# Kernel optimization log

Hardware: AMD Instinct MI355X
Metric: run time of the kernel (lower is better)

Reference implementation:

```python
import jax, jax.numpy as jnp
import numpy as np
from jax import lax

C_DIM = 64
N_HEADS = 8
PATCH = 3
PAD = (PATCH - 1) // 2
EPS = 1e-6


def _unfold(x, p, pad):
    # x: [B,C,H,W] -> [B, C*p*p, H*W], torch.F.unfold ordering (C slowest, then ph, pw)
    B, C, H, W = x.shape
    xp = jnp.pad(x, ((0, 0), (0, 0), (pad, pad), (pad, pad)))
    cols = jnp.stack([xp[:, :, i:i + H, j:j + W] for i in range(p) for j in range(p)], axis=2)
    return cols.reshape(B, C * p * p, H * W)


def _fold(cols, p, pad, H, W):
    # cols: [B, C*p*p, H*W] -> [B,C,H,W] via col2im scatter-add (torch.F.fold)
    B = cols.shape[0]
    C = cols.shape[1] // (p * p)
    cols = cols.reshape(B, C, p * p, H, W)
    out = jnp.zeros((B, C, H + 2 * pad, W + 2 * pad), cols.dtype)
    for i in range(p):
        for j in range(p):
            out = out.at[:, :, i:i + H, j:j + W].add(cols[:, :, i * p + j])
    return out[:, :, pad:pad + H, pad:pad + W]


def _linear_attn(q, k, v):
    # q,k,v: [B, h, N, d]; non-softmax linear attention with ReLU features
    kv = jnp.einsum('bhnd,bhne->bhde', k, v)          # [B,h,d,d]
    ksum = k.sum(axis=2)                              # [B,h,d]
    denom = jnp.einsum('bhnd,bhd->bhn', q, ksum) + EPS
    out = jnp.einsum('bhnd,bhde->bhne', q, kv) / denom[..., None]
    return out


def setup_inputs() -> dict:
    key = jax.random.key(0)
    ks = jax.random.split(key, 5)
    B, C, H, W = 4, C_DIM, 128, 128
    x = jax.random.normal(ks[0], (B, C, H, W), jnp.float32)
    w_qkv = jax.random.normal(ks[1], (3 * C, C), jnp.float32) * 0.05
    b_qkv = jax.random.normal(ks[2], (3 * C,), jnp.float32) * 0.01
    w_proj = jax.random.normal(ks[3], (C, C, 3, 3), jnp.float32) * 0.05
    b_proj = jax.random.normal(ks[4], (C,), jnp.float32) * 0.01
    return {"x": x, "w_qkv": w_qkv, "b_qkv": b_qkv, "w_proj": w_proj, "b_proj": b_proj}


def reference(x, w_qkv, b_qkv, w_proj, b_proj):
    B, C, H, W = x.shape
    p, pad, h = PATCH, PAD, N_HEADS
    N = H * W
    # 1x1 conv qkv
    qkv = jnp.einsum('bchw,oc->bohw', x, w_qkv) + b_qkv[None, :, None, None]
    q, k, v = qkv[:, :C], qkv[:, C:2 * C], qkv[:, 2 * C:]
    q = jax.nn.relu(q)
    k = jax.nn.relu(k)
    # im2col: [B, C*p*p, N]
    qc = _unfold(q, p, pad)
    kc = _unfold(k, p, pad)
    vc = _unfold(v, p, pad)
    d = (C * p * p) // h
    qh = qc.reshape(B, h, d, N).transpose(0, 1, 3, 2)  # [B,h,N,d]
    kh = kc.reshape(B, h, d, N).transpose(0, 1, 3, 2)
    vh = vc.reshape(B, h, d, N).transpose(0, 1, 3, 2)
    o = _linear_attn(qh, kh, vh)                       # [B,h,N,d]
    oc = o.transpose(0, 1, 3, 2).reshape(B, C * p * p, N)
    folded = _fold(oc, p, pad, H, W)
    ones_cols = _unfold(jnp.ones((B, C, H, W), x.dtype), p, pad)
    counts = _fold(ones_cols, p, pad, H, W)
    y = folded / counts
    # 3x3 proj conv
    y = lax.conv_general_dilated(y, w_proj, (1, 1), [(1, 1), (1, 1)],
                                 dimension_numbers=('NCHW', 'OIHW', 'NCHW'))
    y = y + b_proj[None, :, None, None]
    return y
```

## Files before the change

kernel.cpp:

```cpp
#include <hip/hip_runtime.h>

#define BB 4
#define CC 64
#define HH 128
#define WW 128
#define NN (HH*WW)
#define HP 130
#define NPP (HP*HP)
#define HPS 136
#define VROWS 132
#define NPPS (VROWS*HPS)
#define HP2 132
#define NPP2 (HP2*HP2)
#define NH 8
#define DD 72

__global__ __launch_bounds__(256) void k0_wt(const float* __restrict__ wproj, float* __restrict__ wt){
    int idx = blockIdx.x*256 + threadIdx.x;
    if (idx >= 64*9*64) return;
    int oc = idx & 63;
    int w  = (idx >> 6) % 9;
    int ci = idx / 576;
    wt[idx] = wproj[(oc*64 + ci)*9 + w];
}

__global__ __launch_bounds__(256) void k1_qkv(const float* __restrict__ x,
        const float* __restrict__ wqkv, const float* __restrict__ bqkv,
        float* __restrict__ Qp, float* __restrict__ Kp, float* __restrict__ Vp){
    __shared__ float wl[64*68];
    __shared__ float bl[64];
    const int t = threadIdx.x;
    const int gy = blockIdx.y;
    const int b  = blockIdx.z;
    for (int k = 0; k < 16; ++k){
        int idx = t + k*256;
        int orel = idx >> 6, c = idx & 63;
        wl[c*68 + orel] = wqkv[(gy*64 + orel)*64 + c];
    }
    if (t < 64) bl[t] = bqkv[gy*64 + t];
    __syncthreads();
    const int pix = blockIdx.x*256 + t;
    float acc[64];
#pragma unroll
    for (int o=0;o<64;++o) acc[o]=0.f;
    const float* xb = x + (size_t)(b*64)*NN + pix;
    for (int c=0;c<64;++c){
        float xv = xb[(size_t)c*NN];
        const float4* wrow = (const float4*)(&wl[c*68]);
#pragma unroll
        for (int o4=0;o4<16;++o4){
            float4 wv = wrow[o4];
            acc[o4*4+0] += xv*wv.x;
            acc[o4*4+1] += xv*wv.y;
            acc[o4*4+2] += xv*wv.z;
            acc[o4*4+3] += xv*wv.w;
        }
    }
    const int y = pix >> 7, xx = pix & 127;
    float* dst; size_t cstride;
    if (gy == 0){ dst = Qp + (size_t)(b*64)*NPP2 + (y+2)*HP2 + (xx+2); cstride = NPP2; }
    else { dst = ((gy==1)?Kp:Vp) + (size_t)(b*64)*NPPS + (y+2)*HPS + (xx+4); cstride = NPPS; }
    const bool dorelu = (gy < 2);
#pragma unroll
    for (int o=0;o<64;++o){
        float v = acc[o] + bl[o];
        if (dorelu) v = fmaxf(v, 0.f);
        dst[(size_t)o*cstride] = v;
    }
}

__global__ __launch_bounds__(256) void k2_ksum(const float* __restrict__ Kp, float* __restrict__ ksum){
    const int c = blockIdx.x, b = blockIdx.y;
    const float* src = Kp + (size_t)(b*64 + c)*NPPS;
    float a[3][3];
#pragma unroll
    for (int i=0;i<3;++i)
#pragma unroll
        for (int j=0;j<3;++j) a[i][j]=0.f;
    for (int idx = threadIdx.x; idx < NPPS; idx += 256){
        int r = idx / HPS, cc = idx - r*HPS;
        float v = src[idx];
#pragma unroll
        for (int i=0;i<3;++i){
            bool fy = (unsigned)(r - 1 - i) < 128u;
#pragma unroll
            for (int j=0;j<3;++j){
                bool fx = (unsigned)(cc - 3 - j) < 128u;
                if (fy && fx) a[i][j] += v;
            }
        }
    }
    __shared__ float red[4][9];
#pragma unroll
    for (int i=0;i<3;++i)
#pragma unroll
        for (int j=0;j<3;++j){
            float v = a[i][j];
            for (int m=1;m<64;m<<=1) v += __shfl_xor(v, m, 64);
            a[i][j] = v;
        }
    int wave = threadIdx.x >> 6, lane = threadIdx.x & 63;
    if (lane == 0){
#pragma unroll
        for (int w=0;w<9;++w) red[wave][w] = a[w/3][w%3];
    }
    __syncthreads();
    if (threadIdx.x < 9){
        float s = red[0][threadIdx.x]+red[1][threadIdx.x]+red[2][threadIdx.x]+red[3][threadIdx.x];
        int h = c >> 3, cl = c & 7;
        ksum[(b*NH + h)*DD + cl*9 + threadIdx.x] = s;
    }
}

__global__ __launch_bounds__(256) void k3a_corr(const float* __restrict__ Kp, const float* __restrict__ Vp,
                                                float* __restrict__ Cpart){
    const int t = threadIdx.x;
    const int pair = blockIdx.x;
    const int cd = pair >> 3, ce = pair & 7;
    const int h = blockIdx.y, b = blockIdx.z;
    const int bh = b*NH + h;
    const float* Kc = Kp + (size_t)(b*64 + h*8 + cd)*NPPS;
    const float* Vc = Vp + (size_t)(b*64 + h*8 + ce)*NPPS;
    const int x0 = (t & 31) * 4;
    const int yb = t >> 5;
    float C[25];
#pragma unroll
    for (int k=0;k<25;++k) C[k]=0.f;

    for (int it=0; it<16; ++it){
        const int y = yb*16 + it;
        const float* kb = Kc + (y+2)*HPS + 4 + x0;
        float4 kk4 = *(const float4*)kb;
        float kk[4] = {kk4.x, kk4.y, kk4.z, kk4.w};
        const float* vb = Vc + y*HPS + x0;
#pragma unroll
        for (int dr=0; dr<5; ++dr){
            float vv[12];
            const float* vrow = vb + dr*HPS;
#pragma unroll
            for (int q=0;q<3;++q){
                float4 a = *(const float4*)(vrow + 4*q);
                vv[4*q]=a.x; vv[4*q+1]=a.y; vv[4*q+2]=a.z; vv[4*q+3]=a.w;
            }
#pragma unroll
            for (int dj=0; dj<5; ++dj)
#pragma unroll
                for (int p=0; p<4; ++p)
                    C[dr*5+dj] += kk[p] * vv[p+dj+2];
        }
    }
#pragma unroll
    for (int k=0;k<25;++k){
        float v = C[k];
        for (int m=1;m<64;m<<=1) v += __shfl_xor(v, m, 64);
        C[k] = v;
    }
    __shared__ float red[4][25];
    const int wave = t >> 6, lane = t & 63;
    if (lane == 0){
#pragma unroll
        for (int k=0;k<25;++k) red[wave][k] = C[k];
    }
    __syncthreads();
    if (t < 25){
        float s = red[0][t]+red[1][t]+red[2][t]+red[3][t];
        Cpart[((size_t)bh*64 + pair)*25 + t] = s;
    }
}

__global__ __launch_bounds__(128) void k3c_kv(const float* __restrict__ Kp, const float* __restrict__ Vp,
                                              const float* __restrict__ Cpart, float* __restrict__ kvT2){
    __shared__ float Krow[2][136];
    __shared__ float Vrow[10][136];
    __shared__ float Kcol[132][2];
    __shared__ float Vcol[132][16];
    __shared__ float corr[100];
    __shared__ float C25s[25];
    const int t = threadIdx.x;
    const int pair = blockIdx.x;
    const int cd = pair >> 3, ce = pair & 7;
    const int h = blockIdx.y, b = blockIdx.z;
    const int bh = b*NH + h;
    const float* Kc = Kp + (size_t)(b*64 + h*8 + cd)*NPPS;
    const float* Vc = Vp + (size_t)(b*64 + h*8 + ce)*NPPS;
    for (int idx=t; idx<2*136; idx+=128){
        int side = idx/136, col = idx - side*136;
        Krow[side][col] = Kc[(side?129:2)*HPS + col];
    }
    for (int idx=t; idx<10*136; idx+=128){
        int s = idx/136, col = idx - s*136;
        int row = (s<5)? s : (122+s);
        Vrow[s][col] = Vc[row*HPS + col];
    }
    for (int idx=t; idx<132*2; idx+=128){
        int row = idx>>1, side = idx&1;
        Kcol[row][side] = Kc[row*HPS + (side?131:4)];
    }
    for (int idx=t; idx<132*16; idx+=128){
        int row = idx>>4, g = idx&15;
        Vcol[row][g] = Vc[row*HPS + ((g<8)? g : (120+g))];
    }
    __syncthreads();
    if (t < 100){
        int kind = t/50, rem = t%50, side = rem/25, sh = rem%25;
        int di2 = sh/5, dj2 = sh - di2*5;
        float s = 0.f;
        if (kind == 0){
            const float* kr = &Krow[side][4];
            const float* vr = &Vrow[side*5+di2][2+dj2];
            for (int bb=0; bb<128; ++bb) s += kr[bb]*vr[bb];
        } else {
            const int g = side? (9+dj2) : (2+dj2);
            for (int a=0; a<128; ++a) s += Kcol[2+a][side]*Vcol[a+di2][g];
        }
        corr[t] = s;
    } else if (t < 125){
        C25s[t-100] = Cpart[((size_t)bh*64 + pair)*25 + (t-100)];
    }
    __syncthreads();
    if (t < 81){
        int i = t/27, j = (t/9)%3, i2 = (t/3)%3, j2 = t%3;
        int di2 = i2-i+2, dj2 = j2-j+2;
        float val = C25s[di2*5+dj2];
        int si = (i==0)?1:0;
        int sj = (j==0)?1:0;
        if (i != 1) val -= corr[si*25 + di2*5 + dj2];
        if (j != 1) val -= corr[50 + sj*25 + di2*5 + dj2];
        if (i != 1 && j != 1){
            int cj = (j==0)?127:0;
            val += Krow[si][4+cj] * Vrow[si*5+di2][2+cj+dj2];
        }
        kvT2[((size_t)bh*DD + ce*9 + i2*3 + j2)*96 + cd*12 + i*3 + j] = val;
    }
}

__global__ __launch_bounds__(256) void k4_r(const float* __restrict__ Qp, const float* __restrict__ ksum,
                                            float* __restrict__ rfp){
    const int h = blockIdx.y, b = blockIdx.z;
    __shared__ float ks[72];
    if (threadIdx.x < 72) ks[threadIdx.x] = ksum[(b*NH + h)*DD + threadIdx.x];
    __syncthreads();
    const int pix = blockIdx.x*256 + threadIdx.x;
    const int y = pix >> 7, xx = pix & 127;
    const float* Qb = Qp + (size_t)(b*64 + h*8)*NPP2 + (y+1)*HP2 + (xx+1);
    float denom = 0.f;
#pragma unroll
    for (int cl=0; cl<8; ++cl){
        const float* q = Qb + (size_t)cl*NPP2;
#pragma unroll
        for (int w=0; w<9; ++w){
            denom += q[(w/3)*HP2 + (w%3)] * ks[cl*9 + w];
        }
    }
    rfp[(size_t)(b*NH + h)*NPP + (y+1)*HP + (xx+1)] = 1.f/(denom + 1e-6f);
}

__global__ __launch_bounds__(512) void k5_attn(const float* __restrict__ Qp, const float* __restrict__ kvT2,
          const float* __restrict__ rfp, float* __restrict__ folded){
    __shared__ __align__(16) float Qt[8*20*20];
    __shared__ __align__(16) float rt[18*20];
    const int t = threadIdx.x;
    const int tile = blockIdx.x;
    const int h = blockIdx.y, b = blockIdx.z;
    const int ty0 = (tile >> 3)*16, tx0 = (tile & 7)*16;

    const float* Qb = Qp + (size_t)(b*64 + h*8)*NPP2 + (size_t)ty0*HP2 + tx0;
    for (int idx=t; idx<8*20*20; idx+=512){
        int cl = idx / 400; int rem = idx - cl*400; int r = rem/20, cc = rem - r*20;
        Qt[idx] = Qb[(size_t)cl*NPP2 + r*HP2 + cc];
    }
    const float* rg = rfp + (size_t)(b*NH + h)*NPP + (size_t)ty0*HP + tx0;
    for (int idx=t; idx<18*18; idx+=512){
        int rr = idx / 18, cc = idx - rr*18;
        rt[rr*20 + cc] = rg[rr*HP + cc];
    }
    __syncthreads();

    const int c  = __builtin_amdgcn_readfirstlane(t >> 6);
    const int l  = t & 63;
    const int pr = l >> 2;
    const int pc = (l & 3) * 4;

    const float* kvc = kvT2 + ((size_t)(b*NH + h)*DD + c*9)*96;

    float acc[9][4];
#pragma unroll
    for (int u=0;u<9;++u)
#pragma unroll
        for (int p=0;p<4;++p) acc[u][p]=0.f;

    for (int cl=0; cl<8; ++cl){
        float qw[5][8];
        const float* qb = &Qt[cl*400 + pr*20 + pc];
#pragma unroll
        for (int rr=0; rr<5; ++rr){
            float4 a0 = *(const float4*)(qb + rr*20);
            float4 a1 = *(const float4*)(qb + rr*20 + 4);
            qw[rr][0]=a0.x; qw[rr][1]=a0.y; qw[rr][2]=a0.z; qw[rr][3]=a0.w;
            qw[rr][4]=a1.x; qw[rr][5]=a1.y; qw[rr][6]=a1.z; qw[rr][7]=a1.w;
        }
#pragma unroll
        for (int u=0; u<9; ++u){
            const float* kr = kvc + u*96 + cl*12;
            float kw[9];
#pragma unroll
            for (int i=0;i<9;++i) kw[i] = kr[i];
            const int iu = u/3, ju = u - iu*3;
#pragma unroll
            for (int w=0; w<9; ++w){
                const int rr = (w/3) - iu + 2;
                const int cc = (w%3) - ju + 2;
#pragma unroll
                for (int p=0;p<4;++p)
                    acc[u][p] += qw[rr][cc+p] * kw[w];
            }
        }
    }
    float rw[3][6];
    const float* rb = &rt[pr*20 + pc];
#pragma unroll
    for (int rr=0; rr<3; ++rr)
#pragma unroll
        for (int j=0; j<6; ++j) rw[rr][j] = rb[rr*20 + j];
    float out[4];
#pragma unroll
    for (int p=0;p<4;++p) out[p]=0.f;
#pragma unroll
    for (int u=0; u<9; ++u){
        const int iu = u/3, ju = u - iu*3;
#pragma unroll
        for (int p=0;p<4;++p)
            out[p] += acc[u][p] * rw[2-iu][p+2-ju];
    }
    const int iy = ty0 + pr;
    const float ry = 3.f - (float)(iy==0) - (float)(iy==127);
#pragma unroll
    for (int p=0;p<4;++p){
        const int ix = tx0 + pc + p;
        const float rx = 3.f - (float)(ix==0) - (float)(ix==127);
        out[p] = out[p] / (ry*rx);
    }
    float4 o4 = make_float4(out[0], out[1], out[2], out[3]);
    *(float4*)(&folded[(size_t)(b*64 + h*8 + c)*NN + (ty0+pr)*WW + tx0 + pc]) = o4;
}

__global__ __launch_bounds__(512) void k6_conv(const float* __restrict__ folded, const float* __restrict__ wt,
         const float* __restrict__ bproj, float* __restrict__ out){
    __shared__ __align__(16) float ut[64*18*12];
    const int t = threadIdx.x;
    const int tile = blockIdx.x;
    const int b = blockIdx.y;
    const int ty0 = (tile >> 4)*16, tx0 = (tile & 15)*8;

    for (int idx=t; idx<64*18*10; idx+=512){
        int ci = idx / 180; int rem = idx - ci*180; int rr = rem/10, cc = rem - rr*10;
        int iy = ty0 - 1 + rr, ix = tx0 - 1 + cc;
        float v = 0.f;
        if ((unsigned)iy < 128u && (unsigned)ix < 128u)
            v = folded[(size_t)(b*64 + ci)*NN + iy*WW + ix];
        ut[ci*216 + rr*12 + cc] = v;
    }
    __syncthreads();

    const int ocg = t & 31;
    const int s   = t >> 5;
    float acc[2][8];
#pragma unroll
    for (int ol=0;ol<2;++ol)
#pragma unroll
        for (int p=0;p<8;++p) acc[ol][p]=0.f;

    for (int ci=0; ci<64; ++ci){
        float uw[3][10];
        const float* ub = &ut[ci*216 + s*12];
#pragma unroll
        for (int dy=0;dy<3;++dy){
            float4 a0 = *(const float4*)(ub + dy*12);
            float4 a1 = *(const float4*)(ub + dy*12 + 4);
            float2 a2 = *(const float2*)(ub + dy*12 + 8);
            uw[dy][0]=a0.x; uw[dy][1]=a0.y; uw[dy][2]=a0.z; uw[dy][3]=a0.w;
            uw[dy][4]=a1.x; uw[dy][5]=a1.y; uw[dy][6]=a1.z; uw[dy][7]=a1.w;
            uw[dy][8]=a2.x; uw[dy][9]=a2.y;
        }
#pragma unroll
        for (int w=0;w<9;++w){
            const int dy = w/3, dx = w%3;
            float2 wv = *(const float2*)(&wt[(ci*9 + w)*64 + ocg*2]);
#pragma unroll
            for (int p=0;p<8;++p){
                float u = uw[dy][p+dx];
                acc[0][p] += wv.x*u;
                acc[1][p] += wv.y*u;
            }
        }
    }
    const int y = ty0 + s;
    const float2 bias = *(const float2*)(&bproj[ocg*2]);
#pragma unroll
    for (int ol=0;ol<2;++ol){
        const int oc = ocg*2 + ol;
        float* dst = &out[(size_t)(b*64 + oc)*NN + y*WW + tx0];
        const float bv = ol ? bias.y : bias.x;
        float4 v0 = make_float4(acc[ol][0]+bv, acc[ol][1]+bv, acc[ol][2]+bv, acc[ol][3]+bv);
        float4 v1 = make_float4(acc[ol][4]+bv, acc[ol][5]+bv, acc[ol][6]+bv, acc[ol][7]+bv);
        *(float4*)(dst)     = v0;
        *(float4*)(dst + 4) = v1;
    }
}

extern "C" void kernel_launch(void* const* d_in, const int* in_sizes, int n_in,
                              void* d_out, int out_size, void* d_ws, size_t ws_size,
                              hipStream_t stream) {
    const float* x     = (const float*)d_in[0];
    const float* wqkv  = (const float*)d_in[1];
    const float* bqkv  = (const float*)d_in[2];
    const float* wproj = (const float*)d_in[3];
    const float* bproj = (const float*)d_in[4];
    float* out = (float*)d_out;
    float* ws  = (float*)d_ws;

    const size_t szQ2 = (size_t)BB*CC*NPP2;
    const size_t szFS = (size_t)BB*CC*NPPS;
    const size_t szR  = (size_t)BB*NH*NPP;
    const size_t szKV = (size_t)BB*NH*DD*96;
    const size_t szKS = (size_t)BB*NH*DD;
    float* Qp2    = ws;
    float* Kp     = Qp2 + szQ2;
    float* Vp     = Kp + szFS;
    float* rfp    = Vp + szFS;
    float* kvT2   = rfp + szR;
    float* ksum   = kvT2 + szKV;
    float* folded = ksum + szKS;
    float* wt     = folded + (size_t)BB*CC*NN;
    float* Cpart  = folded;

    hipMemsetAsync(ws, 0, (szQ2 + 2*szFS + szR)*sizeof(float), stream);

    k0_wt   <<<dim3(144),      256, 0, stream>>>(wproj, wt);
    k1_qkv  <<<dim3(64, 3, 4), 256, 0, stream>>>(x, wqkv, bqkv, Qp2, Kp, Vp);
    k2_ksum <<<dim3(64, 4),    256, 0, stream>>>(Kp, ksum);
    k3a_corr<<<dim3(64, 8, 4), 256, 0, stream>>>(Kp, Vp, Cpart);
    k3c_kv  <<<dim3(64, 8, 4), 128, 0, stream>>>(Kp, Vp, Cpart, kvT2);
    k4_r    <<<dim3(64, 8, 4), 256, 0, stream>>>(Qp2, ksum, rfp);
    k5_attn <<<dim3(64, 8, 4), 512, 0, stream>>>(Qp2, kvT2, rfp, folded);
    k6_conv <<<dim3(128, 4),   512, 0, stream>>>(folded, wt, bproj, out);
}
```

Measured before the change: 407.9 us.

## Zero only halo pads and reuse V rows in a register window

A bulk memset of the padded Q, K, V and r buffers is replaced by a small kernel that zeroes only the halo rows and columns, so tens of megabytes of memset writes are no longer issued. The correlation kernel now keeps a rolling five-row register window of V, so each row is loaded once instead of five times. This relies on the QKV kernel writing every interior element, and the register window raises register pressure in k3a_corr.

```diff
diff --git a/kernel.cpp b/kernel.cpp
--- a/kernel.cpp
+++ b/kernel.cpp
@@ -15,6 +15,47 @@
 #define NH 8
 #define DD 72
 
+__global__ __launch_bounds__(256) void kz_pads(float* __restrict__ Qp, float* __restrict__ Kp,
+                                               float* __restrict__ rfp){
+    const int t = threadIdx.x;
+    const int c = blockIdx.x;
+    if (c < 256){
+        float* f = Qp + (size_t)c*NPP2;
+        for (int idx=t; idx<4*HP2; idx+=256){
+            int rs = idx / HP2, col = idx - rs*HP2;
+            int row = (rs<2)? rs : (128+rs);
+            f[row*HP2 + col] = 0.f;
+        }
+        for (int idx=t; idx<128*4; idx+=256){
+            int row = 2 + (idx>>2), cs = idx&3;
+            int col = (cs<2)? cs : (128+cs);
+            f[row*HP2 + col] = 0.f;
+        }
+    } else if (c < 768){
+        float* f = Kp + (size_t)(c-256)*NPPS;
+        for (int idx=t; idx<4*HPS; idx+=256){
+            int rs = idx / HPS, col = idx - rs*HPS;
+            int row = (rs<2)? rs : (128+rs);
+            f[row*HPS + col] = 0.f;
+        }
+        for (int idx=t; idx<128*8; idx+=256){
+            int row = 2 + (idx>>3), cs = idx&7;
+            int col = (cs<4)? cs : (128+cs);
+            f[row*HPS + col] = 0.f;
+        }
+    } else {
+        float* f = rfp + (size_t)(c-768)*NPP;
+        for (int idx=t; idx<2*HP; idx+=256){
+            int rs = idx / HP, col = idx - rs*HP;
+            f[(rs?129:0)*HP + col] = 0.f;
+        }
+        for (int idx=t; idx<128*2; idx+=256){
+            int row = 1 + (idx>>1);
+            f[row*HP + ((idx&1)?129:0)] = 0.f;
+        }
+    }
+}
+
 __global__ __launch_bounds__(256) void k0_wt(const float* __restrict__ wproj, float* __restrict__ wt){
     int idx = blockIdx.x*256 + threadIdx.x;
     if (idx >= 64*9*64) return;
@@ -123,30 +164,39 @@
     const float* Vc = Vp + (size_t)(b*64 + h*8 + ce)*NPPS;
     const int x0 = (t & 31) * 4;
     const int yb = t >> 5;
+    const int y0 = yb*16;
     float C[25];
 #pragma unroll
     for (int k=0;k<25;++k) C[k]=0.f;
 
+    float vv[5][12];
+    const float* vbase = Vc + (size_t)y0*HPS + x0;
+#pragma unroll
+    for (int rr=0; rr<4; ++rr){
+#pragma unroll
+        for (int q=0;q<3;++q){
+            float4 a = *(const float4*)(vbase + rr*HPS + 4*q);
+            vv[rr][4*q]=a.x; vv[rr][4*q+1]=a.y; vv[rr][4*q+2]=a.z; vv[rr][4*q+3]=a.w;
+        }
+    }
+#pragma unroll
     for (int it=0; it<16; ++it){
-        const int y = yb*16 + it;
-        const float* kb = Kc + (y+2)*HPS + 4 + x0;
-        float4 kk4 = *(const float4*)kb;
+        const int slot = (it+4)%5;
+#pragma unroll
+        for (int q=0;q<3;++q){
+            float4 a = *(const float4*)(vbase + (it+4)*HPS + 4*q);
+            vv[slot][4*q]=a.x; vv[slot][4*q+1]=a.y; vv[slot][4*q+2]=a.z; vv[slot][4*q+3]=a.w;
+        }
+        float4 kk4 = *(const float4*)(Kc + (size_t)(y0+it+2)*HPS + 4 + x0);
         float kk[4] = {kk4.x, kk4.y, kk4.z, kk4.w};
-        const float* vb = Vc + y*HPS + x0;
 #pragma unroll
         for (int dr=0; dr<5; ++dr){
-            float vv[12];
-            const float* vrow = vb + dr*HPS;
-#pragma unroll
-            for (int q=0;q<3;++q){
-                float4 a = *(const float4*)(vrow + 4*q);
-                vv[4*q]=a.x; vv[4*q+1]=a.y; vv[4*q+2]=a.z; vv[4*q+3]=a.w;
-            }
+            const float* vrow = vv[(it+dr)%5];
 #pragma unroll
             for (int dj=0; dj<5; ++dj)
 #pragma unroll
                 for (int p=0; p<4; ++p)
-                    C[dr*5+dj] += kk[p] * vv[p+dj+2];
+                    C[dr*5+dj] += kk[p] * vrow[p+dj+2];
         }
     }
 #pragma unroll
@@ -434,8 +484,7 @@
     float* wt     = folded + (size_t)BB*CC*NN;
     float* Cpart  = folded;
 
-    hipMemsetAsync(ws, 0, (szQ2 + 2*szFS + szR)*sizeof(float), stream);
-
+    kz_pads <<<dim3(800),      256, 0, stream>>>(Qp2, Kp, rfp);
     k0_wt   <<<dim3(144),      256, 0, stream>>>(wproj, wt);
     k1_qkv  <<<dim3(64, 3, 4), 256, 0, stream>>>(x, wqkv, bqkv, Qp2, Kp, Vp);
     k2_ksum <<<dim3(64, 4),    256, 0, stream>>>(Kp, ksum);
```

After: 361.0 us. -11.5%, faster.
